# Performance work log

Hardware: AMD Instinct MI355X
Metric: run time of the kernel (lower is better)

The kernel has to match this reference:

```python
import jax, jax.numpy as jnp
import numpy as np

EMBED_DIM = 1024
NUM_HEAD = 16
HEAD_DIM = EMBED_DIM // NUM_HEAD
SCALE = HEAD_DIM ** -0.5


def setup_inputs() -> dict:
    key = jax.random.key(0)
    ks = jax.random.split(key, 8)
    B, N, K, D = 2, 2048, 2048, EMBED_DIM
    s = D ** -0.5
    return {
        "x": jax.random.normal(ks[0], (B, N, D), jnp.float32),
        "ctx": jax.random.normal(ks[1], (B, K, D), jnp.float32),
        "Wq": jax.random.normal(ks[2], (D, D), jnp.float32) * s,
        "bq": jnp.zeros((D,), jnp.float32),
        "Wkv": jax.random.normal(ks[3], (D, 2 * D), jnp.float32) * s,
        "bkv": jnp.zeros((2 * D,), jnp.float32),
        "Wproj": jax.random.normal(ks[4], (D, D), jnp.float32) * s,
        "bproj": jnp.zeros((D,), jnp.float32),
    }


def reference(x, ctx, Wq, bq, Wkv, bkv, Wproj, bproj):
    B, N, D = x.shape
    K = ctx.shape[1]
    H, hd = NUM_HEAD, HEAD_DIM
    # Q projection -> [B, H, N, hd]
    q = (x @ Wq + bq).reshape(B, N, H, hd).transpose(0, 2, 1, 3)
    # KV projection -> k, v each [B, H, K, hd]
    kv = (ctx @ Wkv + bkv).reshape(B, K, 2, H, hd).transpose(2, 0, 3, 1, 4)
    k, v = kv[0], kv[1]
    # scaled dot-product attention with materialized scores [B, H, N, K]
    attn = jnp.einsum("bhnd,bhkd->bhnk", q * SCALE, k)
    attn = jax.nn.softmax(attn, axis=-1)
    out = jnp.einsum("bhnk,bhkd->bhnd", attn, v)
    out = out.transpose(0, 2, 1, 3).reshape(B, N, D)
    return out @ Wproj + bproj
```

## Files before the change

### kernel.cpp

```cpp
#include <hip/hip_runtime.h>
#include <hip/hip_bf16.h>

typedef __attribute__((ext_vector_type(8))) short bf16x8;
typedef __attribute__((ext_vector_type(4))) float f32x4;
typedef __attribute__((ext_vector_type(16))) float f32x16;
typedef unsigned short u16;
typedef unsigned int u32;

#define NUM_HEAD 16
#define HEAD_DIM 64
#define SEQ_N 2048
#define SEQ_K 2048
#define EMB 1024
#define MROWS 4096
static constexpr float ATTN_SCALE_LOG2E = 0.125f * 1.44269504f;

#if __has_builtin(__builtin_amdgcn_exp2f)
#define EXP2(x) __builtin_amdgcn_exp2f(x)
#else
#define EXP2(x) __expf(0.69314718056f * (x))
#endif

#if __has_builtin(__builtin_amdgcn_rcpf)
#define RCP(x) __builtin_amdgcn_rcpf(x)
#else
#define RCP(x) (1.0f / (x))
#endif

__device__ __forceinline__ u16 f2bf(float f) {
  __hip_bfloat16 h = __float2bfloat16(f);
  return *reinterpret_cast<u16*>(&h);
}

__device__ __forceinline__ u32 pack2(float lo, float hi) {
  __hip_bfloat162 h = __float22bfloat162_rn(make_float2(lo, hi));
  return *reinterpret_cast<u32*>(&h);
}

__device__ __forceinline__ void plswap(u32& a, u32& b) {
  auto r = __builtin_amdgcn_permlane32_swap(a, b, false, false);
  a = r[0]; b = r[1];
}

__device__ __forceinline__ void async16(const u16* g, u16* l) {
  __builtin_amdgcn_global_load_lds(
      (const __attribute__((address_space(1))) unsigned int*)g,
      (__attribute__((address_space(3))) unsigned int*)l, 16, 0, 0);
}

__global__ __launch_bounds__(256) void cvt2(const float* __restrict__ x,
                                            const float* __restrict__ ctx,
                                            u16* __restrict__ xb, u16* __restrict__ cb) {
  const int n4 = MROWS * EMB / 4;
  int gid = blockIdx.x * 256 + threadIdx.x;
  const float4* s; ushort4* d; int i;
  if (gid < n4) { s = (const float4*)x;   d = (ushort4*)xb; i = gid; }
  else          { s = (const float4*)ctx; d = (ushort4*)cb; i = gid - n4; }
  float4 v = s[i];
  ushort4 o;
  o.x = f2bf(v.x); o.y = f2bf(v.y); o.z = f2bf(v.z); o.w = f2bf(v.w);
  d[i] = o;
}

__global__ __launch_bounds__(256) void transpose_cvt4(
    const float* __restrict__ Wq, const float* __restrict__ Wkv,
    const float* __restrict__ Wproj,
    u16* __restrict__ Wqt, u16* __restrict__ Wkvt, u16* __restrict__ Wpt) {
  __shared__ float tile[32][33];
  const int z = blockIdx.z;
  const float* W; u16* Wt; int srcN, colbase;
  if (z == 0)      { W = Wq;    Wt = Wqt;                          srcN = 1024; colbase = 0; }
  else if (z == 1) { W = Wkv;   Wt = Wkvt;                         srcN = 2048; colbase = 0; }
  else if (z == 2) { W = Wkv;   Wt = Wkvt + (size_t)1024 * 1024;   srcN = 2048; colbase = 1024; }
  else             { W = Wproj; Wt = Wpt;                          srcN = 1024; colbase = 0; }
  int n0 = blockIdx.x * 32, k0 = blockIdx.y * 32;
  int tx = threadIdx.x & 31, ty = threadIdx.x >> 5;
  #pragma unroll
  for (int i = ty; i < 32; i += 8)
    tile[i][tx] = W[(size_t)(k0 + i) * srcN + colbase + n0 + tx];
  __syncthreads();
  #pragma unroll
  for (int i = ty; i < 32; i += 8)
    Wt[(size_t)(n0 + i) * 1024 + k0 + tx] = f2bf(tile[tx][i]);
}

__global__ __launch_bounds__(256, 3) void gemm_qkv(
    const u16* __restrict__ xb, const u16* __restrict__ cb,
    const u16* __restrict__ Wqt, const u16* __restrict__ Wkvt,
    const float* __restrict__ bq, const float* __restrict__ bkv,
    u16* __restrict__ Qb, u16* __restrict__ Kb, u16* __restrict__ Vtb)
{
  __shared__ alignas(16) u16 smem[(128 + 128) * 64];
  u16* As = smem;
  u16* Bs = smem + 128 * 64;
  const int tid = threadIdx.x;
  const bool isQ = (blockIdx.y < 8);
  const int n0 = (isQ ? blockIdx.y : blockIdx.y - 8) * 128;
  const int m0 = blockIdx.x * 128;
  const u16* A      = isQ ? xb : cb;
  const u16* Wt     = isQ ? Wqt : Wkvt;
  const float* bias = isQ ? bq : bkv;
  const int wave = tid >> 6, lane = tid & 63;
  const int wm = (wave >> 1) * 64, wn = (wave & 1) * 64;
  const int l15 = lane & 15, quad = lane >> 4;

  f32x4 acc[4][4];
  #pragma unroll
  for (int i = 0; i < 4; i++)
    #pragma unroll
    for (int j = 0; j < 4; j++)
      #pragma unroll
      for (int r = 0; r < 4; r++) acc[i][j][r] = 0.0f;

  const int srow = tid >> 3;
  const int scol = (tid & 7) * 8;
  const u16* ag = A + (size_t)(m0 + srow) * EMB + scol;
  const u16* bg = Wt + (size_t)(n0 + srow) * EMB + scol;
  const int ldsoff = tid * 8;

  for (int kt = 0; kt < EMB; kt += 64) {
    #pragma unroll
    for (int s = 0; s < 4; s++) {
      async16(ag + (size_t)(s * 32) * EMB + kt, &As[ldsoff + s * 2048]);
      async16(bg + (size_t)(s * 32) * EMB + kt, &Bs[ldsoff + s * 2048]);
    }
    __syncthreads();
    #pragma unroll
    for (int ks = 0; ks < 2; ks++) {
      bf16x8 af[4], bfr[4];
      #pragma unroll
      for (int i = 0; i < 4; i++)
        af[i]  = *(const bf16x8*)&As[(wm + i * 16 + l15) * 64 + ks * 32 + quad * 8];
      #pragma unroll
      for (int j = 0; j < 4; j++)
        bfr[j] = *(const bf16x8*)&Bs[(wn + j * 16 + l15) * 64 + ks * 32 + quad * 8];
      #pragma unroll
      for (int i = 0; i < 4; i++)
        #pragma unroll
        for (int j = 0; j < 4; j++)
          acc[i][j] = __builtin_amdgcn_mfma_f32_16x16x32_bf16(af[i], bfr[j], acc[i][j], 0, 0, 0);
    }
    __syncthreads();
  }

  const int h = ((n0 + wn) >> 6) & 15;
  if (isQ) {
    #pragma unroll
    for (int j = 0; j < 4; j++) {
      const int gc = n0 + wn + j * 16 + l15;
      const float bv = bias[gc];
      const int d = j * 16 + l15;
      #pragma unroll
      for (int i = 0; i < 4; i++) {
        #pragma unroll
        for (int r = 0; r < 4; r++) {
          const int gm = m0 + wm + i * 16 + quad * 4 + r;
          const int bb = gm >> 11, nn = gm & 2047;
          Qb[((size_t)(bb * NUM_HEAD + h) * SEQ_N + nn) * HEAD_DIM + d] =
              f2bf((acc[i][j][r] + bv) * ATTN_SCALE_LOG2E);
        }
      }
    }
  } else if ((n0 >> 10) == 0) {
    #pragma unroll
    for (int j = 0; j < 4; j++) {
      const int gc = n0 + wn + j * 16 + l15;
      const float bv = bias[gc];
      const int d = j * 16 + l15;
      #pragma unroll
      for (int i = 0; i < 4; i++) {
        #pragma unroll
        for (int r = 0; r < 4; r++) {
          const int gm = m0 + wm + i * 16 + quad * 4 + r;
          const int bb = gm >> 11, kk = gm & 2047;
          Kb[((size_t)(bb * NUM_HEAD + h) * SEQ_K + kk) * HEAD_DIM + d] =
              f2bf(acc[i][j][r] + bv);
        }
      }
    }
  } else {
    u16* wbuf = smem + wave * 1088;
    const int gm0 = m0 + wm;
    const int bb = gm0 >> 11;
    const int kk0 = gm0 & 2047;
    #pragma unroll
    for (int j = 0; j < 4; j++) {
      const int gc = n0 + wn + j * 16 + l15;
      const float bv = bias[gc];
      #pragma unroll
      for (int i = 0; i < 4; i++) {
        ushort4 pk;
        pk.x = f2bf(acc[i][j][0] + bv);
        pk.y = f2bf(acc[i][j][1] + bv);
        pk.z = f2bf(acc[i][j][2] + bv);
        pk.w = f2bf(acc[i][j][3] + bv);
        *(ushort4*)&wbuf[l15 * 68 + i * 16 + quad * 4] = pk;
      }
      #pragma unroll
      for (int it = 0; it < 2; it++) {
        const int dd = it * 8 + (lane >> 3);
        const int kp = (lane & 7) * 8;
        uint4 v = *(const uint4*)&wbuf[dd * 68 + kp];
        *(uint4*)(Vtb + ((size_t)(bb * NUM_HEAD + h) * HEAD_DIM + j * 16 + dd) * SEQ_K
                  + kk0 + kp) = v;
      }
    }
  }
}

__global__ __launch_bounds__(256) void gemm_proj(
    const u16* __restrict__ A, const u16* __restrict__ Wt,
    const float* __restrict__ bias, float* __restrict__ outF)
{
  __shared__ alignas(16) u16 smem[(64 + 128) * 64];
  u16* As = smem;
  u16* Bs = smem + 64 * 64;
  const int tid = threadIdx.x;
  const int n0 = blockIdx.y * 128, m0 = blockIdx.x * 64;
  const int wave = tid >> 6, lane = tid & 63;
  const int wm = (wave >> 1) * 32, wn = (wave & 1) * 64;
  const int l15 = lane & 15, quad = lane >> 4;

  f32x4 acc[2][4];
  #pragma unroll
  for (int i = 0; i < 2; i++)
    #pragma unroll
    for (int j = 0; j < 4; j++)
      #pragma unroll
      for (int r = 0; r < 4; r++) acc[i][j][r] = 0.0f;

  const int srow = tid >> 3;
  const int scol = (tid & 7) * 8;
  const u16* ag = A + (size_t)(m0 + srow) * EMB + scol;
  const u16* bg = Wt + (size_t)(n0 + srow) * EMB + scol;
  const int ldsoff = tid * 8;

  for (int kt = 0; kt < EMB; kt += 64) {
    async16(ag + kt, &As[ldsoff]);
    async16(ag + (size_t)32 * EMB + kt, &As[ldsoff + 2048]);
    #pragma unroll
    for (int s = 0; s < 4; s++)
      async16(bg + (size_t)(s * 32) * EMB + kt, &Bs[ldsoff + s * 2048]);
    __syncthreads();
    #pragma unroll
    for (int ks = 0; ks < 2; ks++) {
      bf16x8 af[2], bfr[4];
      #pragma unroll
      for (int i = 0; i < 2; i++)
        af[i]  = *(const bf16x8*)&As[(wm + i * 16 + l15) * 64 + ks * 32 + quad * 8];
      #pragma unroll
      for (int j = 0; j < 4; j++)
        bfr[j] = *(const bf16x8*)&Bs[(wn + j * 16 + l15) * 64 + ks * 32 + quad * 8];
      #pragma unroll
      for (int i = 0; i < 2; i++)
        #pragma unroll
        for (int j = 0; j < 4; j++)
          acc[i][j] = __builtin_amdgcn_mfma_f32_16x16x32_bf16(af[i], bfr[j], acc[i][j], 0, 0, 0);
    }
    __syncthreads();
  }

  #pragma unroll
  for (int i = 0; i < 2; i++) {
    #pragma unroll
    for (int j = 0; j < 4; j++) {
      const int gc = n0 + wn + j * 16 + l15;
      const float bv = bias[gc];
      #pragma unroll
      for (int r = 0; r < 4; r++) {
        const int gm = m0 + wm + i * 16 + quad * 4 + r;
        outF[(size_t)gm * EMB + gc] = acc[i][j][r] + bv;
      }
    }
  }
}

__global__ __launch_bounds__(256, 2) void attn_kernel(
    const u16* __restrict__ Qb, const u16* __restrict__ Kb,
    const u16* __restrict__ Vtb, u16* __restrict__ Ob)
{
  __shared__ alignas(16) u16 Ks[2][128 * 64];
  __shared__ alignas(16) u16 Vs[2][64 * 128];
  const int tid = threadIdx.x;
  const int bh = blockIdx.x;
  const int m0 = blockIdx.y * 128;
  const int wave = tid >> 6, lane = tid & 63;
  const int l31 = lane & 31, hi = lane >> 5;
  const int hi16 = hi * 16;
  const int swzK = (l31 & 7) << 4;
  const int swzV = (l31 & 15) << 4;
  const int rowb = m0 + wave * 32;

  bf16x8 bq[4];
  {
    const u16* qp = Qb + ((size_t)bh * SEQ_N + rowb + l31) * HEAD_DIM + hi * 8;
    #pragma unroll
    for (int db = 0; db < 4; db++) bq[db] = *(const bf16x8*)(qp + db * 16);
  }

  f32x16 o0, o1, od;
  #pragma unroll
  for (int r = 0; r < 16; r++) { o0[r] = 0.f; o1[r] = 0.f; od[r] = 0.f; }
  f32x16 zc;
  #pragma unroll
  for (int r = 0; r < 16; r++) zc[r] = 0.f;
  union { u32 u[4]; bf16x8 v; } ones;
  ones.u[0] = ones.u[1] = ones.u[2] = ones.u[3] = 0x3F803F80u;

  const int krow0 = tid >> 3;
  const int ksg   = (tid & 7) ^ (krow0 & 7);
  const int vrow0 = tid >> 4;
  const int vsg   = (tid & 15) ^ vrow0;
  const u16* kg = Kb  + (size_t)bh * SEQ_K * HEAD_DIM;
  const u16* vg = Vtb + (size_t)bh * HEAD_DIM * SEQ_K;

#define STAGE(kt_, nb_) do {                                                   \
    _Pragma("unroll")                                                          \
    for (int s = 0; s < 4; s++) {                                              \
      async16(kg + (size_t)((kt_) + s * 32 + krow0) * HEAD_DIM + ksg * 8,      \
              &Ks[nb_][s * 2048 + tid * 8]);                                   \
      async16(vg + (size_t)(s * 16 + vrow0) * SEQ_K + (kt_) + vsg * 8,         \
              &Vs[nb_][s * 2048 + tid * 8]);                                   \
    }                                                                          \
  } while (0)

  STAGE(0, 0);
  __syncthreads();

  for (int kt = 0; kt < SEQ_K; kt += 128) {
    const int cur = (kt >> 7) & 1;
    if (kt + 128 < SEQ_K) STAGE(kt + 128, cur ^ 1);
    const char* KsB = (const char*)Ks[cur];
    const char* VsB = (const char*)Vs[cur];

    #pragma unroll
    for (int g = 0; g < 4; g++) {
      __builtin_amdgcn_s_setprio(1);
      bf16x8 ka = *(const bf16x8*)(KsB + (g * 32 + l31) * 128 + (hi16 ^ swzK));
      f32x16 s = __builtin_amdgcn_mfma_f32_32x32x16_bf16(ka, bq[0], zc, 0, 0, 0);
      #pragma unroll
      for (int db = 1; db < 4; db++) {
        ka = *(const bf16x8*)(KsB + (g * 32 + l31) * 128 + ((db * 32 + hi16) ^ swzK));
        s = __builtin_amdgcn_mfma_f32_32x32x16_bf16(ka, bq[db], s, 0, 0, 0);
      }
      __builtin_amdgcn_s_setprio(0);

      float p[16];
      #pragma unroll
      for (int r = 0; r < 16; r++) p[r] = EXP2(s[r]);
      u32 w0 = pack2(p[0],  p[1]),  w1 = pack2(p[2],  p[3]);
      u32 w2 = pack2(p[4],  p[5]),  w3 = pack2(p[6],  p[7]);
      u32 w4 = pack2(p[8],  p[9]),  w5 = pack2(p[10], p[11]);
      u32 w6 = pack2(p[12], p[13]), w7 = pack2(p[14], p[15]);
      plswap(w0, w2); plswap(w1, w3);
      plswap(w4, w6); plswap(w5, w7);
      union PU { u32 u[4]; bf16x8 v; } pa0, pa1;
      pa0.u[0] = w0; pa0.u[1] = w1; pa0.u[2] = w2; pa0.u[3] = w3;
      pa1.u[0] = w4; pa1.u[1] = w5; pa1.u[2] = w6; pa1.u[3] = w7;

      __builtin_amdgcn_s_setprio(1);
      bf16x8 vb00 = *(const bf16x8*)(VsB + (l31)*256      + ((g * 64 + hi16)      ^ swzV));
      bf16x8 vb01 = *(const bf16x8*)(VsB + (l31)*256      + ((g * 64 + 32 + hi16) ^ swzV));
      bf16x8 vb10 = *(const bf16x8*)(VsB + (32 + l31)*256 + ((g * 64 + hi16)      ^ swzV));
      bf16x8 vb11 = *(const bf16x8*)(VsB + (32 + l31)*256 + ((g * 64 + 32 + hi16) ^ swzV));
      o0 = __builtin_amdgcn_mfma_f32_32x32x16_bf16(pa0.v, vb00, o0, 0, 0, 0);
      o1 = __builtin_amdgcn_mfma_f32_32x32x16_bf16(pa0.v, vb10, o1, 0, 0, 0);
      od = __builtin_amdgcn_mfma_f32_32x32x16_bf16(pa0.v, ones.v, od, 0, 0, 0);
      o0 = __builtin_amdgcn_mfma_f32_32x32x16_bf16(pa1.v, vb01, o0, 0, 0, 0);
      o1 = __builtin_amdgcn_mfma_f32_32x32x16_bf16(pa1.v, vb11, o1, 0, 0, 0);
      od = __builtin_amdgcn_mfma_f32_32x32x16_bf16(pa1.v, ones.v, od, 0, 0, 0);
      __builtin_amdgcn_s_setprio(0);
    }
    __syncthreads();
  }
#undef STAGE

  const int bb = bh >> 4, hh = bh & 15;
  #pragma unroll
  for (int r = 0; r < 16; r++) {
    const int qrow = (r & 3) + 8 * (r >> 2) + 4 * hi;
    const float invr = RCP(od[r]);
    const int gm = rowb + qrow;
    u16* op = Ob + ((size_t)bb * SEQ_N + gm) * EMB + hh * HEAD_DIM + l31;
    op[0]  = f2bf(o0[r] * invr);
    op[32] = f2bf(o1[r] * invr);
  }
}

extern "C" void kernel_launch(void* const* d_in, const int* in_sizes, int n_in,
                              void* d_out, int out_size, void* d_ws, size_t ws_size,
                              hipStream_t stream)
{
  const float* x     = (const float*)d_in[0];
  const float* ctx   = (const float*)d_in[1];
  const float* Wq    = (const float*)d_in[2];
  const float* bq    = (const float*)d_in[3];
  const float* Wkv   = (const float*)d_in[4];
  const float* bkv   = (const float*)d_in[5];
  const float* Wproj = (const float*)d_in[6];
  const float* bproj = (const float*)d_in[7];
  float* out = (float*)d_out;

  char* ws = (char*)d_ws;
  size_t off = 0;
  auto walloc = [&](size_t bytes) -> void* {
    void* p = ws + off;
    off += (bytes + 255) & ~(size_t)255;
    return p;
  };
  u16* xb   = (u16*)walloc((size_t)MROWS * EMB * 2);
  u16* cb   = (u16*)walloc((size_t)MROWS * EMB * 2);
  u16* Wqt  = (u16*)walloc((size_t)EMB * EMB * 2);
  u16* Wkvt = (u16*)walloc((size_t)2 * EMB * EMB * 2);
  u16* Wpt  = (u16*)walloc((size_t)EMB * EMB * 2);
  u16* Qb   = (u16*)walloc((size_t)MROWS * EMB * 2);
  u16* Kb   = (u16*)walloc((size_t)MROWS * EMB * 2);
  u16* Vtb  = (u16*)walloc((size_t)MROWS * EMB * 2);
  u16* Ob   = (u16*)walloc((size_t)MROWS * EMB * 2);

  cvt2<<<8192, 256, 0, stream>>>(x, ctx, xb, cb);
  transpose_cvt4<<<dim3(32, 32, 4), 256, 0, stream>>>(Wq, Wkv, Wproj, Wqt, Wkvt, Wpt);
  gemm_qkv<<<dim3(32, 24), 256, 0, stream>>>(xb, cb, Wqt, Wkvt, bq, bkv, Qb, Kb, Vtb);
  attn_kernel<<<dim3(32, 16), 256, 0, stream>>>(Qb, Kb, Vtb, Ob);
  gemm_proj<<<dim3(64, 8), 256, 0, stream>>>(Ob, Wpt, bproj, out);
}
```

Before: 203.8 us.

## Software-pipeline QK^T of next group with softmax of current group in attention

Restructures the inner attention loop so the QK^T MFMAs for the next 32-key group are issued while the exp2/pack/permlane work for the current group runs, using two score accumulators in ping-pong. Sched group barriers interleave LDS reads, MFMAs and VALU ops, and the setprio hints are removed. The aim is to hide the transcendental and packing latency behind matrix-core work, at the cost of extra accumulator registers that could lower occupancy or cause spills.

Result: no change. 202.8 us (-0.5%).

```diff
diff --git a/kernel.cpp b/kernel.cpp
--- a/kernel.cpp
+++ b/kernel.cpp
@@ -26,6 +26,8 @@
 #else
 #define RCP(x) (1.0f / (x))
 #endif
+
+#define SGB __builtin_amdgcn_sched_group_barrier
 
 __device__ __forceinline__ u16 f2bf(float f) {
   __hip_bfloat16 h = __float2bfloat16(f);
@@ -324,6 +326,16 @@
     }                                                                          \
   } while (0)
 
+#define QKGRP(gg, dst) do {                                                    \
+    bf16x8 ka_ = *(const bf16x8*)(KsB + ((gg) * 32 + l31) * 128 + (hi16 ^ swzK)); \
+    dst = __builtin_amdgcn_mfma_f32_32x32x16_bf16(ka_, bq[0], zc, 0, 0, 0);    \
+    _Pragma("unroll")                                                          \
+    for (int db = 1; db < 4; db++) {                                           \
+      ka_ = *(const bf16x8*)(KsB + ((gg) * 32 + l31) * 128 + ((db * 32 + hi16) ^ swzK)); \
+      dst = __builtin_amdgcn_mfma_f32_32x32x16_bf16(ka_, bq[db], dst, 0, 0, 0); \
+    }                                                                          \
+  } while (0)
+
   STAGE(0, 0);
   __syncthreads();
 
@@ -333,21 +345,24 @@
     const char* KsB = (const char*)Ks[cur];
     const char* VsB = (const char*)Vs[cur];
 
+    f32x16 sA, sB;
+    QKGRP(0, sA);
+
     #pragma unroll
     for (int g = 0; g < 4; g++) {
-      __builtin_amdgcn_s_setprio(1);
-      bf16x8 ka = *(const bf16x8*)(KsB + (g * 32 + l31) * 128 + (hi16 ^ swzK));
-      f32x16 s = __builtin_amdgcn_mfma_f32_32x32x16_bf16(ka, bq[0], zc, 0, 0, 0);
-      #pragma unroll
-      for (int db = 1; db < 4; db++) {
-        ka = *(const bf16x8*)(KsB + (g * 32 + l31) * 128 + ((db * 32 + hi16) ^ swzK));
-        s = __builtin_amdgcn_mfma_f32_32x32x16_bf16(ka, bq[db], s, 0, 0, 0);
-      }
-      __builtin_amdgcn_s_setprio(0);
+      f32x16& sc = (g & 1) ? sB : sA;
+      f32x16& sn = (g & 1) ? sA : sB;
+
+      bf16x8 vb00 = *(const bf16x8*)(VsB + (l31)*256      + ((g * 64 + hi16)      ^ swzV));
+      bf16x8 vb01 = *(const bf16x8*)(VsB + (l31)*256      + ((g * 64 + 32 + hi16) ^ swzV));
+      bf16x8 vb10 = *(const bf16x8*)(VsB + (32 + l31)*256 + ((g * 64 + hi16)      ^ swzV));
+      bf16x8 vb11 = *(const bf16x8*)(VsB + (32 + l31)*256 + ((g * 64 + 32 + hi16) ^ swzV));
+
+      if (g < 3) QKGRP(g + 1, sn);
 
       float p[16];
       #pragma unroll
-      for (int r = 0; r < 16; r++) p[r] = EXP2(s[r]);
+      for (int r = 0; r < 16; r++) p[r] = EXP2(sc[r]);
       u32 w0 = pack2(p[0],  p[1]),  w1 = pack2(p[2],  p[3]);
       u32 w2 = pack2(p[4],  p[5]),  w3 = pack2(p[6],  p[7]);
       u32 w4 = pack2(p[8],  p[9]),  w5 = pack2(p[10], p[11]);
@@ -358,21 +373,23 @@
       pa0.u[0] = w0; pa0.u[1] = w1; pa0.u[2] = w2; pa0.u[3] = w3;
       pa1.u[0] = w4; pa1.u[1] = w5; pa1.u[2] = w6; pa1.u[3] = w7;
 
-      __builtin_amdgcn_s_setprio(1);
-      bf16x8 vb00 = *(const bf16x8*)(VsB + (l31)*256      + ((g * 64 + hi16)      ^ swzV));
-      bf16x8 vb01 = *(const bf16x8*)(VsB + (l31)*256      + ((g * 64 + 32 + hi16) ^ swzV));
-      bf16x8 vb10 = *(const bf16x8*)(VsB + (32 + l31)*256 + ((g * 64 + hi16)      ^ swzV));
-      bf16x8 vb11 = *(const bf16x8*)(VsB + (32 + l31)*256 + ((g * 64 + 32 + hi16) ^ swzV));
       o0 = __builtin_amdgcn_mfma_f32_32x32x16_bf16(pa0.v, vb00, o0, 0, 0, 0);
       o1 = __builtin_amdgcn_mfma_f32_32x32x16_bf16(pa0.v, vb10, o1, 0, 0, 0);
       od = __builtin_amdgcn_mfma_f32_32x32x16_bf16(pa0.v, ones.v, od, 0, 0, 0);
       o0 = __builtin_amdgcn_mfma_f32_32x32x16_bf16(pa1.v, vb01, o0, 0, 0, 0);
       o1 = __builtin_amdgcn_mfma_f32_32x32x16_bf16(pa1.v, vb11, o1, 0, 0, 0);
       od = __builtin_amdgcn_mfma_f32_32x32x16_bf16(pa1.v, ones.v, od, 0, 0, 0);
-      __builtin_amdgcn_s_setprio(0);
+
+      SGB(0x100, 8, 0);
+      SGB(0x008, 2, 0);
+      SGB(0x002, 24, 0);
+      SGB(0x008, 2, 0);
+      SGB(0x002, 24, 0);
+      SGB(0x008, 6, 0);
     }
     __syncthreads();
   }
+#undef QKGRP
 #undef STAGE
 
   const int bb = bh >> 4, hh = bh & 15;
```

## Split attention over two key halves and combine partial outputs in projection GEMM

Applied to the files above, without the earlier changes.

The attention kernel now splits the key sequence into two halves along a new grid dimension. This doubles the block count and uses smaller 64-row K/V tiles so more blocks can fit per CU. Each half writes unnormalized fp32 partial outputs and row sums. The projection GEMM loads both partials, adds them, normalizes, converts to bf16 and stores into shared memory, replacing the async bf16 load. The two conversion kernels are also merged into one launch. The trade-off is much more intermediate fp32 traffic and synchronous A-tile loads in the projection GEMM.

New measurement: 219.6 us. +7.8%, slower.

```diff
diff --git a/kernel.cpp b/kernel.cpp
--- a/kernel.cpp
+++ b/kernel.cpp
@@ -48,32 +48,34 @@
       (__attribute__((address_space(3))) unsigned int*)l, 16, 0, 0);
 }
 
-__global__ __launch_bounds__(256) void cvt2(const float* __restrict__ x,
-                                            const float* __restrict__ ctx,
-                                            u16* __restrict__ xb, u16* __restrict__ cb) {
-  const int n4 = MROWS * EMB / 4;
-  int gid = blockIdx.x * 256 + threadIdx.x;
-  const float4* s; ushort4* d; int i;
-  if (gid < n4) { s = (const float4*)x;   d = (ushort4*)xb; i = gid; }
-  else          { s = (const float4*)ctx; d = (ushort4*)cb; i = gid - n4; }
-  float4 v = s[i];
-  ushort4 o;
-  o.x = f2bf(v.x); o.y = f2bf(v.y); o.z = f2bf(v.z); o.w = f2bf(v.w);
-  d[i] = o;
-}
-
-__global__ __launch_bounds__(256) void transpose_cvt4(
+__global__ __launch_bounds__(256) void cvt_all(
+    const float* __restrict__ x, const float* __restrict__ ctx,
     const float* __restrict__ Wq, const float* __restrict__ Wkv,
     const float* __restrict__ Wproj,
+    u16* __restrict__ xb, u16* __restrict__ cb,
     u16* __restrict__ Wqt, u16* __restrict__ Wkvt, u16* __restrict__ Wpt) {
   __shared__ float tile[32][33];
-  const int z = blockIdx.z;
+  const int bid = blockIdx.x;
+  if (bid < 8192) {
+    const int n4 = MROWS * EMB / 4;
+    int gid = bid * 256 + threadIdx.x;
+    const float4* s; ushort4* d; int i;
+    if (gid < n4) { s = (const float4*)x;   d = (ushort4*)xb; i = gid; }
+    else          { s = (const float4*)ctx; d = (ushort4*)cb; i = gid - n4; }
+    float4 v = s[i];
+    ushort4 o;
+    o.x = f2bf(v.x); o.y = f2bf(v.y); o.z = f2bf(v.z); o.w = f2bf(v.w);
+    d[i] = o;
+    return;
+  }
+  const int tb = bid - 8192;
+  const int z = tb >> 10;
   const float* W; u16* Wt; int srcN, colbase;
   if (z == 0)      { W = Wq;    Wt = Wqt;                          srcN = 1024; colbase = 0; }
   else if (z == 1) { W = Wkv;   Wt = Wkvt;                         srcN = 2048; colbase = 0; }
   else if (z == 2) { W = Wkv;   Wt = Wkvt + (size_t)1024 * 1024;   srcN = 2048; colbase = 1024; }
   else             { W = Wproj; Wt = Wpt;                          srcN = 1024; colbase = 0; }
-  int n0 = blockIdx.x * 32, k0 = blockIdx.y * 32;
+  int n0 = (tb & 31) * 32, k0 = ((tb >> 5) & 31) * 32;
   int tx = threadIdx.x & 31, ty = threadIdx.x >> 5;
   #pragma unroll
   for (int i = ty; i < 32; i += 8)
@@ -209,7 +211,9 @@
 }
 
 __global__ __launch_bounds__(256) void gemm_proj(
-    const u16* __restrict__ A, const u16* __restrict__ Wt,
+    const float* __restrict__ Oa, const float* __restrict__ Obp,
+    const float* __restrict__ Da, const float* __restrict__ Dbp,
+    const u16* __restrict__ Wt,
     const float* __restrict__ bias, float* __restrict__ outF)
 {
   __shared__ alignas(16) u16 smem[(64 + 128) * 64];
@@ -231,16 +235,30 @@
 
   const int srow = tid >> 3;
   const int scol = (tid & 7) * 8;
-  const u16* ag = A + (size_t)(m0 + srow) * EMB + scol;
   const u16* bg = Wt + (size_t)(n0 + srow) * EMB + scol;
   const int ldsoff = tid * 8;
 
   for (int kt = 0; kt < EMB; kt += 64) {
-    async16(ag + kt, &As[ldsoff]);
-    async16(ag + (size_t)32 * EMB + kt, &As[ldsoff + 2048]);
     #pragma unroll
     for (int s = 0; s < 4; s++)
       async16(bg + (size_t)(s * 32) * EMB + kt, &Bs[ldsoff + s * 2048]);
+    const int hh = kt >> 6;
+    #pragma unroll
+    for (int s = 0; s < 2; s++) {
+      const int grow = m0 + srow + s * 32;
+      const float inv = RCP(Da[grow * 16 + hh] + Dbp[grow * 16 + hh]);
+      const float4 a0 = *(const float4*)&Oa [(size_t)grow * EMB + kt + scol];
+      const float4 a1 = *(const float4*)&Oa [(size_t)grow * EMB + kt + scol + 4];
+      const float4 b0 = *(const float4*)&Obp[(size_t)grow * EMB + kt + scol];
+      const float4 b1 = *(const float4*)&Obp[(size_t)grow * EMB + kt + scol + 4];
+      ushort4 p0, p1;
+      p0.x = f2bf((a0.x + b0.x) * inv); p0.y = f2bf((a0.y + b0.y) * inv);
+      p0.z = f2bf((a0.z + b0.z) * inv); p0.w = f2bf((a0.w + b0.w) * inv);
+      p1.x = f2bf((a1.x + b1.x) * inv); p1.y = f2bf((a1.y + b1.y) * inv);
+      p1.z = f2bf((a1.z + b1.z) * inv); p1.w = f2bf((a1.w + b1.w) * inv);
+      *(ushort4*)&As[ldsoff + s * 2048]     = p0;
+      *(ushort4*)&As[ldsoff + s * 2048 + 4] = p1;
+    }
     __syncthreads();
     #pragma unroll
     for (int ks = 0; ks < 2; ks++) {
@@ -275,20 +293,24 @@
   }
 }
 
-__global__ __launch_bounds__(256, 2) void attn_kernel(
+__global__ __launch_bounds__(256, 4) void attn_kernel(
     const u16* __restrict__ Qb, const u16* __restrict__ Kb,
-    const u16* __restrict__ Vtb, u16* __restrict__ Ob)
+    const u16* __restrict__ Vtb,
+    float* __restrict__ Op0, float* __restrict__ Op1, float* __restrict__ Dp0)
 {
-  __shared__ alignas(16) u16 Ks[2][128 * 64];
-  __shared__ alignas(16) u16 Vs[2][64 * 128];
+  __shared__ alignas(16) u16 Ks[2][64 * 64];
+  __shared__ alignas(16) u16 Vs[2][64 * 64];
   const int tid = threadIdx.x;
   const int bh = blockIdx.x;
   const int m0 = blockIdx.y * 128;
+  const int kh = blockIdx.z;
+  const int kbase = kh << 10;
+  float* Op = kh ? Op1 : Op0;
+  float* Dp = Dp0 + (size_t)kh * MROWS * NUM_HEAD;
   const int wave = tid >> 6, lane = tid & 63;
   const int l31 = lane & 31, hi = lane >> 5;
   const int hi16 = hi * 16;
-  const int swzK = (l31 & 7) << 4;
-  const int swzV = (l31 & 15) << 4;
+  const int swz = (l31 & 7) << 4;
   const int rowb = m0 + wave * 32;
 
   bf16x8 bq[4];
@@ -307,40 +329,38 @@
   union { u32 u[4]; bf16x8 v; } ones;
   ones.u[0] = ones.u[1] = ones.u[2] = ones.u[3] = 0x3F803F80u;
 
-  const int krow0 = tid >> 3;
-  const int ksg   = (tid & 7) ^ (krow0 & 7);
-  const int vrow0 = tid >> 4;
-  const int vsg   = (tid & 15) ^ vrow0;
+  const int srow = tid >> 3;
+  const int sgx  = (tid & 7) ^ (srow & 7);
   const u16* kg = Kb  + (size_t)bh * SEQ_K * HEAD_DIM;
   const u16* vg = Vtb + (size_t)bh * HEAD_DIM * SEQ_K;
 
 #define STAGE(kt_, nb_) do {                                                   \
     _Pragma("unroll")                                                          \
-    for (int s = 0; s < 4; s++) {                                              \
-      async16(kg + (size_t)((kt_) + s * 32 + krow0) * HEAD_DIM + ksg * 8,      \
+    for (int s = 0; s < 2; s++) {                                              \
+      async16(kg + (size_t)((kt_) + s * 32 + srow) * HEAD_DIM + sgx * 8,       \
               &Ks[nb_][s * 2048 + tid * 8]);                                   \
-      async16(vg + (size_t)(s * 16 + vrow0) * SEQ_K + (kt_) + vsg * 8,         \
+      async16(vg + (size_t)(s * 32 + srow) * SEQ_K + (kt_) + sgx * 8,          \
               &Vs[nb_][s * 2048 + tid * 8]);                                   \
     }                                                                          \
   } while (0)
 
-  STAGE(0, 0);
+  STAGE(kbase, 0);
   __syncthreads();
 
-  for (int kt = 0; kt < SEQ_K; kt += 128) {
-    const int cur = (kt >> 7) & 1;
-    if (kt + 128 < SEQ_K) STAGE(kt + 128, cur ^ 1);
+  for (int kt = 0; kt < 1024; kt += 64) {
+    const int cur = (kt >> 6) & 1;
+    if (kt + 64 < 1024) STAGE(kbase + kt + 64, cur ^ 1);
     const char* KsB = (const char*)Ks[cur];
     const char* VsB = (const char*)Vs[cur];
 
     #pragma unroll
-    for (int g = 0; g < 4; g++) {
+    for (int g = 0; g < 2; g++) {
       __builtin_amdgcn_s_setprio(1);
-      bf16x8 ka = *(const bf16x8*)(KsB + (g * 32 + l31) * 128 + (hi16 ^ swzK));
+      bf16x8 ka = *(const bf16x8*)(KsB + (g * 32 + l31) * 128 + (hi16 ^ swz));
       f32x16 s = __builtin_amdgcn_mfma_f32_32x32x16_bf16(ka, bq[0], zc, 0, 0, 0);
       #pragma unroll
       for (int db = 1; db < 4; db++) {
-        ka = *(const bf16x8*)(KsB + (g * 32 + l31) * 128 + ((db * 32 + hi16) ^ swzK));
+        ka = *(const bf16x8*)(KsB + (g * 32 + l31) * 128 + ((db * 32 + hi16) ^ swz));
         s = __builtin_amdgcn_mfma_f32_32x32x16_bf16(ka, bq[db], s, 0, 0, 0);
       }
       __builtin_amdgcn_s_setprio(0);
@@ -359,10 +379,10 @@
       pa1.u[0] = w4; pa1.u[1] = w5; pa1.u[2] = w6; pa1.u[3] = w7;
 
       __builtin_amdgcn_s_setprio(1);
-      bf16x8 vb00 = *(const bf16x8*)(VsB + (l31)*256      + ((g * 64 + hi16)      ^ swzV));
-      bf16x8 vb01 = *(const bf16x8*)(VsB + (l31)*256      + ((g * 64 + 32 + hi16) ^ swzV));
-      bf16x8 vb10 = *(const bf16x8*)(VsB + (32 + l31)*256 + ((g * 64 + hi16)      ^ swzV));
-      bf16x8 vb11 = *(const bf16x8*)(VsB + (32 + l31)*256 + ((g * 64 + 32 + hi16) ^ swzV));
+      bf16x8 vb00 = *(const bf16x8*)(VsB + (l31)*128      + ((g * 64 + hi16)      ^ swz));
+      bf16x8 vb01 = *(const bf16x8*)(VsB + (l31)*128      + ((g * 64 + 32 + hi16) ^ swz));
+      bf16x8 vb10 = *(const bf16x8*)(VsB + (32 + l31)*128 + ((g * 64 + hi16)      ^ swz));
+      bf16x8 vb11 = *(const bf16x8*)(VsB + (32 + l31)*128 + ((g * 64 + 32 + hi16) ^ swz));
       o0 = __builtin_amdgcn_mfma_f32_32x32x16_bf16(pa0.v, vb00, o0, 0, 0, 0);
       o1 = __builtin_amdgcn_mfma_f32_32x32x16_bf16(pa0.v, vb10, o1, 0, 0, 0);
       od = __builtin_amdgcn_mfma_f32_32x32x16_bf16(pa0.v, ones.v, od, 0, 0, 0);
@@ -379,11 +399,11 @@
   #pragma unroll
   for (int r = 0; r < 16; r++) {
     const int qrow = (r & 3) + 8 * (r >> 2) + 4 * hi;
-    const float invr = RCP(od[r]);
-    const int gm = rowb + qrow;
-    u16* op = Ob + ((size_t)bb * SEQ_N + gm) * EMB + hh * HEAD_DIM + l31;
-    op[0]  = f2bf(o0[r] * invr);
-    op[32] = f2bf(o1[r] * invr);
+    const size_t grow = (size_t)bb * SEQ_N + (rowb + qrow);
+    float* op = Op + grow * EMB + hh * HEAD_DIM + l31;
+    op[0]  = o0[r];
+    op[32] = o1[r];
+    if (l31 == 0) Dp[grow * 16 + hh] = od[r];
   }
 }
 
@@ -416,11 +436,14 @@
   u16* Qb   = (u16*)walloc((size_t)MROWS * EMB * 2);
   u16* Kb   = (u16*)walloc((size_t)MROWS * EMB * 2);
   u16* Vtb  = (u16*)walloc((size_t)MROWS * EMB * 2);
-  u16* Ob   = (u16*)walloc((size_t)MROWS * EMB * 2);
-
-  cvt2<<<8192, 256, 0, stream>>>(x, ctx, xb, cb);
-  transpose_cvt4<<<dim3(32, 32, 4), 256, 0, stream>>>(Wq, Wkv, Wproj, Wqt, Wkvt, Wpt);
+  float* Opart0 = (float*)xb;
+  float* Opart1 = (float*)walloc((size_t)MROWS * EMB * 4);
+  float* Dpart  = (float*)walloc((size_t)2 * MROWS * NUM_HEAD * 4);
+  float* Dpart1 = Dpart + (size_t)MROWS * NUM_HEAD;
+
+  cvt_all<<<12288, 256, 0, stream>>>(x, ctx, Wq, Wkv, Wproj, xb, cb, Wqt, Wkvt, Wpt);
   gemm_qkv<<<dim3(32, 24), 256, 0, stream>>>(xb, cb, Wqt, Wkvt, bq, bkv, Qb, Kb, Vtb);
-  attn_kernel<<<dim3(32, 16), 256, 0, stream>>>(Qb, Kb, Vtb, Ob);
-  gemm_proj<<<dim3(64, 8), 256, 0, stream>>>(Ob, Wpt, bproj, out);
-}
+  attn_kernel<<<dim3(32, 16, 2), 256, 0, stream>>>(Qb, Kb, Vtb, Opart0, Opart1, Dpart);
+  gemm_proj<<<dim3(64, 8), 256, 0, stream>>>(Opart0, Opart1, Dpart, Dpart1,
+                                             Wpt, bproj, out);
+}
```
